# Kernel optimization log

Hardware: AMD Instinct MI355X
Metric: run time of the kernel (lower is better)

The kernel has to match this reference:

```python
import jax, jax.numpy as jnp
import numpy as np

N_HEADS = 8
N_LEVELS = 1
N_POINTS = 4
D_MODEL = 256
BATCH = 2
H0, W0 = 100, 150
LS = H0 * W0
LQ = 15000


def layer_norm(x, g, b, eps=1e-5):
    m = jnp.mean(x, -1, keepdims=True)
    v = jnp.var(x, -1, keepdims=True)
    return (x - m) * jax.lax.rsqrt(v + eps) * g + b


def bilinear_sample(v, Hl, Wl, loc):
    # v: [N, Hl*Wl, Hh, D] level features; loc in [0,1]: [N, Lq, Hh, P, 2] (x, y)
    Nb, _, Hh, D = v.shape
    Lq, P = loc.shape[1], loc.shape[3]
    x = loc[..., 0] * Wl - 0.5           # align_corners=False grid_sample convention
    y = loc[..., 1] * Hl - 0.5
    x0 = jnp.floor(x); y0 = jnp.floor(y)
    lx = (x - x0).transpose(0, 2, 1, 3)[..., None]   # [N,Hh,Lq,P,1]
    ly = (y - y0).transpose(0, 2, 1, 3)[..., None]
    x0i = x0.astype(jnp.int32); y0i = y0.astype(jnp.int32)
    vh = v.transpose(0, 2, 1, 3)                      # [N,Hh,Hl*Wl,D]

    def gather(xi, yi):
        valid = (xi >= 0) & (xi < Wl) & (yi >= 0) & (yi < Hl)   # zero padding
        idx = jnp.clip(yi, 0, Hl - 1) * Wl + jnp.clip(xi, 0, Wl - 1)
        idxf = idx.transpose(0, 2, 1, 3).reshape(Nb, Hh, Lq * P)
        g = jnp.take_along_axis(vh, idxf[..., None], axis=2).reshape(Nb, Hh, Lq, P, D)
        return g * valid.transpose(0, 2, 1, 3)[..., None]

    g00 = gather(x0i, y0i)
    g10 = gather(x0i + 1, y0i)
    g01 = gather(x0i, y0i + 1)
    g11 = gather(x0i + 1, y0i + 1)
    return (g00 * (1 - lx) * (1 - ly) + g10 * lx * (1 - ly)
            + g01 * (1 - lx) * ly + g11 * lx * ly)   # [N,Hh,Lq,P,D]


def ms_deform_attn(q, reference_points, src, shapes_np, starts_np, padding_mask,
                   W_val, b_val, W_off, b_off, W_attn, b_attn, W_out, b_out):
    Nb, Lq, C = q.shape
    Hh, D, L, P = N_HEADS, C // N_HEADS, N_LEVELS, N_POINTS
    value = src @ W_val + b_val
    value = jnp.where(padding_mask[..., None], 0.0, value).reshape(Nb, -1, Hh, D)
    offsets = (q @ W_off + b_off).reshape(Nb, Lq, Hh, L, P, 2)
    aw = jax.nn.softmax((q @ W_attn + b_attn).reshape(Nb, Lq, Hh, L * P), -1)
    aw = aw.reshape(Nb, Lq, Hh, L, P)
    # offset normalizer is (W, H) per level
    norm = jnp.asarray(shapes_np[:, ::-1].copy(), dtype=q.dtype)   # [L,2]
    loc = reference_points[:, :, None, :, None, :] + offsets / norm[None, None, None, :, None, :]
    out = 0.0
    for l in range(L):
        Hl, Wl = int(shapes_np[l, 0]), int(shapes_np[l, 1])
        s = int(starts_np[l])
        sampled = bilinear_sample(value[:, s:s + Hl * Wl], Hl, Wl, loc[:, :, :, l])
        out = out + jnp.sum(sampled * aw[:, :, :, l].transpose(0, 2, 1, 3)[..., None], axis=3)
    out = out.transpose(0, 2, 1, 3).reshape(Nb, Lq, C)
    return out @ W_out + b_out


def reference(tgt, query_pos, src_pos, tgt_spatial_shapes, reference_points,
              depth_reference_points, src, src_spatial_shapes, frame_start_index,
              src_padding_mask,
              W_dsa, b_dsa, g_nds, b_nds, W_off, b_off, W_attn, b_attn,
              W_val, b_val, W_out, b_out, W_csa, b_csa, g_n1, b_n1,
              W_ff, b_ff, g_n3, b_n3):
    ss = np.asarray(src_spatial_shapes)      # static level shapes
    starts = np.asarray(frame_start_index)
    # depth scale adaptation
    src_a = layer_norm(src @ W_dsa + b_dsa, g_nds, b_nds)
    q = tgt + query_pos
    tgt2 = ms_deform_attn(q, reference_points, src_a, ss, starts, src_padding_mask,
                          W_val, b_val, W_off, b_off, W_attn, b_attn, W_out, b_out)
    tgt2 = tgt2 @ W_csa + b_csa
    t = layer_norm(tgt + tgt2, g_n1, b_n1)
    # FFN: single linear d_model->d_model with exact GELU (per source code)
    ff = jax.nn.gelu(t @ W_ff + b_ff, approximate=False)
    return layer_norm(t + ff, g_n3, b_n3)


def setup_inputs() -> dict:
    key = jax.random.key(0)
    ks = jax.random.split(key, 24)
    C = D_MODEL
    Hh, L, P = N_HEADS, N_LEVELS, N_POINTS

    def lin(k, fin, fout, scale=None):
        s = (1.0 / np.sqrt(fin)) if scale is None else scale
        return (jax.random.normal(k, (fin, fout), jnp.float32) * s).astype(jnp.float32)

    inp = {}
    inp['tgt'] = jax.random.normal(ks[0], (BATCH, LQ, C), jnp.float32)
    inp['query_pos'] = 0.1 * jax.random.normal(ks[1], (BATCH, LQ, C), jnp.float32)
    inp['src_pos'] = 0.1 * jax.random.normal(ks[2], (BATCH, LS, C), jnp.float32)
    inp['tgt_spatial_shapes'] = jnp.array([[H0, W0]], jnp.int32)
    inp['reference_points'] = jax.random.uniform(ks[3], (BATCH, LQ, L, 2), jnp.float32)
    inp['depth_reference_points'] = jax.random.uniform(ks[4], (BATCH, LQ, 1, 2), jnp.float32)
    inp['src'] = jax.random.normal(ks[5], (BATCH, LS, C), jnp.float32)
    inp['src_spatial_shapes'] = jnp.array([[H0, W0]], jnp.int32)
    inp['frame_start_index'] = jnp.array([0], jnp.int32)
    inp['src_padding_mask'] = jnp.zeros((BATCH, LS), jnp.bool_)
    # parameters
    inp['W_dsa'] = lin(ks[6], C, C); inp['b_dsa'] = jnp.zeros((C,), jnp.float32)
    inp['g_nds'] = jnp.ones((C,), jnp.float32); inp['b_nds'] = jnp.zeros((C,), jnp.float32)
    inp['W_off'] = lin(ks[7], C, Hh * L * P * 2, scale=0.01)
    inp['b_off'] = 0.5 * jax.random.normal(ks[8], (Hh * L * P * 2,), jnp.float32)
    inp['W_attn'] = lin(ks[9], C, Hh * L * P)
    inp['b_attn'] = jnp.zeros((Hh * L * P,), jnp.float32)
    inp['W_val'] = lin(ks[10], C, C); inp['b_val'] = jnp.zeros((C,), jnp.float32)
    inp['W_out'] = lin(ks[11], C, C); inp['b_out'] = jnp.zeros((C,), jnp.float32)
    inp['W_csa'] = lin(ks[12], C, C); inp['b_csa'] = jnp.zeros((C,), jnp.float32)
    inp['g_n1'] = jnp.ones((C,), jnp.float32); inp['b_n1'] = jnp.zeros((C,), jnp.float32)
    inp['W_ff'] = lin(ks[13], C, C); inp['b_ff'] = jnp.zeros((C,), jnp.float32)
    inp['g_n3'] = jnp.ones((C,), jnp.float32); inp['b_n3'] = jnp.zeros((C,), jnp.float32)
    return inp
```

## Files before the change

### kernel.cpp

```cpp
#include <hip/hip_runtime.h>
#include <hip/hip_bf16.h>
#include <math.h>

#define LQ   15000
#define LS_  15000
#define NB   2
#define ROWS (NB*LQ)
#define HGT  100
#define WID  150

typedef __attribute__((ext_vector_type(8))) short bf16x8;
typedef __attribute__((ext_vector_type(4))) float f32x4;

__device__ inline short f2bf(float x) {
    __hip_bfloat16 h = __float2bfloat16(x);
    return *reinterpret_cast<short*>(&h);
}
__device__ inline unsigned pack2bf(float a, float b) {
    return ((unsigned)(unsigned short)f2bf(a)) | (((unsigned)(unsigned short)f2bf(b)) << 16);
}
__device__ inline float bf2f(short s) {
    return __uint_as_float(((unsigned)(unsigned short)s) << 16);
}
__device__ inline float gelu_exact(float x) {
    return 0.5f * x * (1.f + erff(x * 0.70710678118654752440f));
}

#if defined(__has_builtin)
#if __has_builtin(__builtin_amdgcn_global_load_lds)
#define HAS_GLL 1
#endif
#endif
#ifndef HAS_GLL
#define HAS_GLL 0
#endif

typedef unsigned int u32;

__device__ __forceinline__ void gld_lds16(const void* g, void* l) {
#if HAS_GLL
    __builtin_amdgcn_global_load_lds(
        (const __attribute__((address_space(1))) u32*)g,
        (__attribute__((address_space(3))) u32*)l,
        16, 0, 0);
#else
    int lane = threadIdx.x & 63;
    *(int4*)((char*)l + lane * 16) = *(const int4*)g;
#endif
}

#if HAS_GLL
#define WAIT_PREV() asm volatile("s_waitcnt vmcnt(4)" ::: "memory")
#define WAIT_LAST() asm volatile("s_waitcnt vmcnt(0)" ::: "memory")
#else
#define WAIT_PREV() asm volatile("s_waitcnt vmcnt(0) lgkmcnt(0)" ::: "memory")
#define WAIT_LAST() asm volatile("s_waitcnt vmcnt(0) lgkmcnt(0)" ::: "memory")
#endif

template<int MODE>
__global__ __launch_bounds__(256, 2) void fused2(
    const void* __restrict__ Ap,
    const short* __restrict__ W1T, const float* __restrict__ bias1,
    const float* __restrict__ res1,
    const float* __restrict__ g1v, const float* __restrict__ b1v,
    const short* __restrict__ W2T, const float* __restrict__ bias2,
    void* __restrict__ Out,
    const unsigned char* __restrict__ mask,
    const float* __restrict__ g2v, const float* __restrict__ b2v,
    int M)
{
    __shared__ __align__(16) char lds[2 * 16384 + 64 * 264 * 2];
    short (*T)[264] = (short(*)[264])(lds + 32768);

    const int tid = threadIdx.x;
    const int bm0 = blockIdx.x * 64;
    const int wave = tid >> 6, lane = tid & 63;
    const int quad = lane >> 4, c = lane & 15;

    const int roff = c * 64 + ((quad ^ ((c >> 1) & 3)) << 4);

    auto stageB = [&](int buf, const short* __restrict__ W, int k0) {
        #pragma unroll
        for (int it = 0; it < 4; ++it) {
            int s = it * 256 + wave * 64 + lane;
            int n = s >> 2;
            int j = (s & 3) ^ ((n >> 1) & 3);
            gld_lds16(W + (size_t)n * 256 + k0 + j * 8,
                      lds + buf * 16384 + (it * 256 + wave * 64) * 16);
        }
    };

    int rA = bm0 + wave * 16 + c; if (rA > M - 1) rA = M - 1;
    bf16x8 aReg[8];

    if (MODE == 1) {
        const short* A = (const short*)Ap + (size_t)rA * 256 + quad * 8;
        #pragma unroll
        for (int k = 0; k < 8; ++k) aReg[k] = *(const bf16x8*)(A + k * 32);
    } else {
        const float* A = (const float*)Ap + (size_t)rA * 256 + quad * 8;
        float4 lo[8], hi[8];
        #pragma unroll
        for (int k = 0; k < 8; ++k) {
            lo[k] = *(const float4*)(A + k * 32);
            hi[k] = *(const float4*)(A + k * 32 + 4);
        }
        #pragma unroll
        for (int k = 0; k < 8; ++k) {
            union { int4 i; bf16x8 v; } u;
            u.i.x = pack2bf(lo[k].x, lo[k].y);
            u.i.y = pack2bf(lo[k].z, lo[k].w);
            u.i.z = pack2bf(hi[k].x, hi[k].y);
            u.i.w = pack2bf(hi[k].z, hi[k].w);
            aReg[k] = u.v;
        }
    }

    stageB(0, W1T, 0);
    stageB(1, W1T, 32);

    f32x4 acc[16];
    #pragma unroll
    for (int t = 0; t < 16; ++t) acc[t] = (f32x4){0.f, 0.f, 0.f, 0.f};

    #pragma unroll
    for (int k = 0; k < 8; ++k) {
        if (k < 7) { WAIT_PREV(); } else { WAIT_LAST(); }
        __builtin_amdgcn_s_barrier();
        const char* bb = lds + (k & 1) * 16384 + roff;
        bf16x8 a = aReg[k];
        #pragma unroll
        for (int t = 0; t < 16; ++t) {
            bf16x8 b = *(const bf16x8*)(bb + t * 1024);
            acc[t] = __builtin_amdgcn_mfma_f32_16x16x32_bf16(a, b, acc[t], 0, 0, 0);
        }
        asm volatile("" ::: "memory");
        __builtin_amdgcn_s_barrier();
        if (k < 6) stageB(k & 1, W1T, (k + 2) * 32);
    }

    stageB(0, W2T, 0);
    stageB(1, W2T, 32);

    float tres[4][16];
    {
        const int rb = wave * 16 + quad * 4;
        #pragma unroll
        for (int reg = 0; reg < 4; ++reg) {
            int rloc = rb + reg;
            int rg = bm0 + rloc; int rgl = (rg < M) ? rg : (M - 1);
            float s = 0.f, sq = 0.f;
            float vv[16];
            #pragma unroll
            for (int t = 0; t < 16; ++t) {
                int col = t * 16 + c;
                float v = acc[t][reg] + bias1[col];
                if (MODE == 1) v += res1[(size_t)rgl * 256 + col];
                vv[t] = v; s += v; sq += v * v;
            }
            #pragma unroll
            for (int o = 1; o < 16; o <<= 1) {
                s += __shfl_xor(s, o, 64); sq += __shfl_xor(sq, o, 64);
            }
            float mean = s * (1.f / 256.f);
            float var  = sq * (1.f / 256.f) - mean * mean;
            float rs   = rsqrtf(var + 1e-5f);
            #pragma unroll
            for (int t = 0; t < 16; ++t) {
                int col = t * 16 + c;
                float ln = (vv[t] - mean) * rs * g1v[col] + b1v[col];
                if (MODE == 1) tres[reg][t] = ln;
                T[rloc][col] = f2bf(ln);
            }
        }
    }

    #pragma unroll
    for (int k = 0; k < 8; ++k)
        aReg[k] = *(const bf16x8*)&T[wave * 16 + c][k * 32 + quad * 8];

    #pragma unroll
    for (int t = 0; t < 16; ++t) acc[t] = (f32x4){0.f, 0.f, 0.f, 0.f};

    #pragma unroll
    for (int k = 0; k < 8; ++k) {
        if (k < 7) { WAIT_PREV(); } else { WAIT_LAST(); }
        __builtin_amdgcn_s_barrier();
        const char* bb = lds + (k & 1) * 16384 + roff;
        bf16x8 a = aReg[k];
        #pragma unroll
        for (int t = 0; t < 16; ++t) {
            bf16x8 b = *(const bf16x8*)(bb + t * 1024);
            acc[t] = __builtin_amdgcn_mfma_f32_16x16x32_bf16(a, b, acc[t], 0, 0, 0);
        }
        asm volatile("" ::: "memory");
        __builtin_amdgcn_s_barrier();
        if (k < 6) stageB(k & 1, W2T, (k + 2) * 32);
    }

    const int rb = wave * 16 + quad * 4;
    if constexpr (MODE == 0) {
        short* O = (short*)Out;
        #pragma unroll
        for (int reg = 0; reg < 4; ++reg) {
            int rloc = rb + reg; int r = bm0 + rloc;
            if (r < M) {
                float mz = mask[r] ? 0.f : 1.f;
                int n = (r >= LS_) ? 1 : 0;
                int sidx = r - n * LS_;
                #pragma unroll
                for (int t = 0; t < 16; ++t) {
                    int col = t * 16 + c; int h = col >> 5, d = col & 31;
                    O[(((size_t)n * 8 + h) * LS_ + sidx) * 32 + d] =
                        f2bf((acc[t][reg] + bias2[col]) * mz);
                }
            }
        }
    } else {
        float* O = (float*)Out;
        #pragma unroll
        for (int reg = 0; reg < 4; ++reg) {
            int r = bm0 + rb + reg;
            float s = 0.f, sq = 0.f;
            float vv[16];
            #pragma unroll
            for (int t = 0; t < 16; ++t) {
                int col = t * 16 + c;
                float v = gelu_exact(acc[t][reg] + bias2[col]) + tres[reg][t];
                vv[t] = v; s += v; sq += v * v;
            }
            #pragma unroll
            for (int o = 1; o < 16; o <<= 1) {
                s += __shfl_xor(s, o, 64); sq += __shfl_xor(sq, o, 64);
            }
            float mean = s * (1.f / 256.f);
            float var  = sq * (1.f / 256.f) - mean * mean;
            float rs   = rsqrtf(var + 1e-5f);
            if (r < M) {
                #pragma unroll
                for (int t = 0; t < 16; ++t) {
                    int col = t * 16 + c;
                    O[(size_t)r * 256 + col] = (vv[t] - mean) * rs * g2v[col] + b2v[col];
                }
            }
        }
    }
}

__global__ __launch_bounds__(256) void oa_gemm(
    const float* __restrict__ tgt, const float* __restrict__ qpos,
    const short* __restrict__ WToa, const float* __restrict__ b_oa,
    float* __restrict__ S_oa, int M)
{
    __shared__ __align__(16) short Bs[96][264];
    __shared__ float sb[96];

    const int tid = threadIdx.x;
    const int bm0 = blockIdx.x * 64;
    const int wave = tid >> 6, lane = tid & 63;
    const int quad = lane >> 4, c = lane & 15;

    if (tid < 96) sb[tid] = b_oa[tid];

    #pragma unroll
    for (int it = 0; it < 12; ++it) {
        int f = it * 256 + tid;
        int n = f >> 5, ko = (f & 31) * 8;
        *(int4*)&Bs[n][ko] = *(const int4*)&WToa[(size_t)n * 256 + ko];
    }

    int r = bm0 + wave * 16 + c; if (r > M - 1) r = M - 1;
    const float* At = tgt  + (size_t)r * 256 + quad * 8;
    const float* Aq = qpos + (size_t)r * 256 + quad * 8;
    bf16x8 aReg[8];
    #pragma unroll
    for (int k = 0; k < 8; ++k) {
        float4 t0 = *(const float4*)(At + k * 32);
        float4 t1 = *(const float4*)(At + k * 32 + 4);
        float4 q0 = *(const float4*)(Aq + k * 32);
        float4 q1 = *(const float4*)(Aq + k * 32 + 4);
        union { int4 i; bf16x8 v; } u;
        u.i.x = pack2bf(t0.x + q0.x, t0.y + q0.y);
        u.i.y = pack2bf(t0.z + q0.z, t0.w + q0.w);
        u.i.z = pack2bf(t1.x + q1.x, t1.y + q1.y);
        u.i.w = pack2bf(t1.z + q1.z, t1.w + q1.w);
        aReg[k] = u.v;
    }

    f32x4 acc[6];
    #pragma unroll
    for (int t = 0; t < 6; ++t) acc[t] = (f32x4){0.f, 0.f, 0.f, 0.f};

    __syncthreads();

    #pragma unroll
    for (int k = 0; k < 8; ++k) {
        bf16x8 a = aReg[k];
        #pragma unroll
        for (int t = 0; t < 6; ++t) {
            bf16x8 b = *(const bf16x8*)&Bs[t * 16 + c][k * 32 + quad * 8];
            acc[t] = __builtin_amdgcn_mfma_f32_16x16x32_bf16(a, b, acc[t], 0, 0, 0);
        }
    }

    const int rb = wave * 16 + quad * 4;
    #pragma unroll
    for (int reg = 0; reg < 4; ++reg) {
        int rr = bm0 + rb + reg;
        if (rr < M) {
            #pragma unroll
            for (int t = 0; t < 6; ++t)
                S_oa[(size_t)rr * 96 + t * 16 + c] = acc[t][reg] + sb[t * 16 + c];
        }
    }
}

__global__ __launch_bounds__(256) void deform_sample(
    const short* __restrict__ value,
    const float* __restrict__ S_oa,
    const float* __restrict__ refp,
    short* __restrict__ out)
{
    int grp = blockIdx.x * 32 + (threadIdx.x >> 3);
    int c4  = threadIdx.x & 7;
    int h = grp & 7;
    int r = grp >> 3;
    int n = (r >= LS_) ? 1 : 0;

    const float* row = S_oa + (size_t)r * 96;
    float rx = refp[(size_t)r * 2 + 0], ry = refp[(size_t)r * 2 + 1];
    float4 oA = *(const float4*)&row[h * 8];
    float4 oB = *(const float4*)&row[h * 8 + 4];
    float4 lg = *(const float4*)&row[64 + h * 4];

    float mx = fmaxf(fmaxf(lg.x, lg.y), fmaxf(lg.z, lg.w));
    float e0 = expf(lg.x - mx), e1 = expf(lg.y - mx), e2 = expf(lg.z - mx), e3 = expf(lg.w - mx);
    float inv = 1.f / (e0 + e1 + e2 + e3);
    float aw[4] = {e0 * inv, e1 * inv, e2 * inv, e3 * inv};
    float ox[4] = {oA.x, oA.z, oB.x, oB.z};
    float oy[4] = {oA.y, oA.w, oB.y, oB.w};

    const short* vb = value + (((size_t)n * 8 + h) * LS_) * 32 + c4 * 4;
    float a0 = 0.f, a1 = 0.f, a2 = 0.f, a3 = 0.f;

    #pragma unroll
    for (int p = 0; p < 4; ++p) {
        float x = rx * (float)WID + ox[p] - 0.5f;
        float y = ry * (float)HGT + oy[p] - 0.5f;
        float x0f = floorf(x), y0f = floorf(y);
        float lx = x - x0f, ly = y - y0f;
        int x0 = (int)x0f, y0 = (int)y0f;
        int x1 = x0 + 1, y1 = y0 + 1;
        bool vx0 = (x0 >= 0) & (x0 < WID), vx1 = (x1 >= 0) & (x1 < WID);
        bool vy0 = (y0 >= 0) & (y0 < HGT), vy1 = (y1 >= 0) & (y1 < HGT);
        float w00 = (vx0 & vy0) ? (1.f - lx) * (1.f - ly) * aw[p] : 0.f;
        float w10 = (vx1 & vy0) ? lx * (1.f - ly) * aw[p] : 0.f;
        float w01 = (vx0 & vy1) ? (1.f - lx) * ly * aw[p] : 0.f;
        float w11 = (vx1 & vy1) ? lx * ly * aw[p] : 0.f;
        int xc0 = min(max(x0, 0), WID - 1), xc1 = min(max(x1, 0), WID - 1);
        int yc0 = min(max(y0, 0), HGT - 1), yc1 = min(max(y1, 0), HGT - 1);
        int2 v00 = *(const int2*)&vb[(size_t)(yc0 * WID + xc0) * 32];
        int2 v10 = *(const int2*)&vb[(size_t)(yc0 * WID + xc1) * 32];
        int2 v01 = *(const int2*)&vb[(size_t)(yc1 * WID + xc0) * 32];
        int2 v11 = *(const int2*)&vb[(size_t)(yc1 * WID + xc1) * 32];
        a0 += w00 * __uint_as_float(((unsigned)v00.x) << 16)
            + w10 * __uint_as_float(((unsigned)v10.x) << 16)
            + w01 * __uint_as_float(((unsigned)v01.x) << 16)
            + w11 * __uint_as_float(((unsigned)v11.x) << 16);
        a1 += w00 * __uint_as_float(v00.x & 0xffff0000u)
            + w10 * __uint_as_float(v10.x & 0xffff0000u)
            + w01 * __uint_as_float(v01.x & 0xffff0000u)
            + w11 * __uint_as_float(v11.x & 0xffff0000u);
        a2 += w00 * __uint_as_float(((unsigned)v00.y) << 16)
            + w10 * __uint_as_float(((unsigned)v10.y) << 16)
            + w01 * __uint_as_float(((unsigned)v01.y) << 16)
            + w11 * __uint_as_float(((unsigned)v11.y) << 16);
        a3 += w00 * __uint_as_float(v00.y & 0xffff0000u)
            + w10 * __uint_as_float(v10.y & 0xffff0000u)
            + w01 * __uint_as_float(v01.y & 0xffff0000u)
            + w11 * __uint_as_float(v11.y & 0xffff0000u);
    }
    int2 o;
    o.x = pack2bf(a0, a1);
    o.y = pack2bf(a2, a3);
    *(int2*)&out[(size_t)r * 256 + h * 32 + c4 * 4] = o;
}

__global__ __launch_bounds__(256) void prep_all(
    const float* __restrict__ W_dsa, const float* __restrict__ W_val,
    const float* __restrict__ W_ff,  const float* __restrict__ W_out,
    const float* __restrict__ W_csa, const float* __restrict__ b_out,
    const float* __restrict__ b_csa, const float* __restrict__ W_off,
    const float* __restrict__ W_attn, const float* __restrict__ b_off,
    const float* __restrict__ b_attn,
    short* __restrict__ WT_dsa, short* __restrict__ WT_val, short* __restrict__ WT_ff,
    short* __restrict__ WT_c, float* __restrict__ bc,
    short* __restrict__ WT_oa, float* __restrict__ b_oa)
{
    __shared__ float tile[64][65];
    const int b = blockIdx.x, tid = threadIdx.x;
    if (b < 48) {
        const float* W = (b < 16) ? W_dsa : (b < 32) ? W_val : W_ff;
        short* WT = (b < 16) ? WT_dsa : (b < 32) ? WT_val : WT_ff;
        int t = b & 15; int bx = (t & 3) * 64, by = (t >> 2) * 64;
        #pragma unroll
        for (int it = 0; it < 4; ++it) {
            int f = it * 256 + tid; int i = f >> 4; int j = (f & 15) * 4;
            float4 v = *(const float4*)&W[(size_t)(by + i) * 256 + bx + j];
            tile[i][j] = v.x; tile[i][j + 1] = v.y; tile[i][j + 2] = v.z; tile[i][j + 3] = v.w;
        }
        __syncthreads();
        #pragma unroll
        for (int it = 0; it < 16; ++it) {
            int f = it * 256 + tid; int nl = f >> 6; int kl = f & 63;
            WT[(size_t)(bx + nl) * 256 + by + kl] = f2bf(tile[kl][nl]);
        }
    } else if (b < 304) {
        int k = b - 48, n = tid;
        float s = 0.f;
        #pragma unroll 8
        for (int j = 0; j < 256; ++j)
            s = fmaf(W_out[(size_t)k * 256 + j], W_csa[(size_t)j * 256 + n], s);
        WT_c[(size_t)n * 256 + k] = f2bf(s);
    } else if (b == 304) {
        int j = tid;
        float s = b_csa[j];
        #pragma unroll 8
        for (int k = 0; k < 256; ++k)
            s = fmaf(b_out[k], W_csa[(size_t)k * 256 + j], s);
        bc[j] = s;
    } else {
        int j = b - 305, k = tid;
        float v = (j < 64) ? W_off[(size_t)k * 64 + j] : W_attn[(size_t)k * 32 + (j - 64)];
        WT_oa[(size_t)j * 256 + k] = f2bf(v);
        if (k == 0) b_oa[j] = (j < 64) ? b_off[j] : b_attn[j - 64];
    }
}

extern "C" void kernel_launch(void* const* d_in, const int* in_sizes, int n_in,
                              void* d_out, int out_size, void* d_ws, size_t ws_size,
                              hipStream_t stream)
{
    const float* tgt       = (const float*)d_in[0];
    const float* query_pos = (const float*)d_in[1];
    const float* refp      = (const float*)d_in[4];
    const float* src       = (const float*)d_in[6];
    const unsigned char* mask = (const unsigned char*)d_in[9];
    const float* W_dsa  = (const float*)d_in[10]; const float* b_dsa  = (const float*)d_in[11];
    const float* g_nds  = (const float*)d_in[12]; const float* b_nds  = (const float*)d_in[13];
    const float* W_off  = (const float*)d_in[14]; const float* b_off  = (const float*)d_in[15];
    const float* W_attn = (const float*)d_in[16]; const float* b_attn = (const float*)d_in[17];
    const float* W_val  = (const float*)d_in[18]; const float* b_val  = (const float*)d_in[19];
    const float* W_out  = (const float*)d_in[20]; const float* b_out  = (const float*)d_in[21];
    const float* W_csa  = (const float*)d_in[22]; const float* b_csa  = (const float*)d_in[23];
    const float* g_n1   = (const float*)d_in[24]; const float* b_n1   = (const float*)d_in[25];
    const float* W_ff   = (const float*)d_in[26]; const float* b_ff   = (const float*)d_in[27];
    const float* g_n3   = (const float*)d_in[28]; const float* b_n3   = (const float*)d_in[29];
    float* out = (float*)d_out;

    short* attn_out = (short*)d_ws;
    short* value    = attn_out + (size_t)ROWS * 256;
    float* S_oa     = (float*)(value + (size_t)ROWS * 256);
    short* WT_dsa   = (short*)(S_oa + (size_t)ROWS * 96);
    short* WT_val   = WT_dsa + 65536;
    short* WT_ff    = WT_val + 65536;
    short* WT_c     = WT_ff + 65536;
    short* WT_oa    = WT_c + 65536;
    float* bc       = (float*)(WT_oa + 96 * 256);
    float* b_oa     = bc + 256;

    dim3 blk(256);
    const int GB = (ROWS + 63) / 64;

    prep_all<<<401, blk, 0, stream>>>(
        W_dsa, W_val, W_ff, W_out, W_csa, b_out, b_csa, W_off, W_attn, b_off, b_attn,
        WT_dsa, WT_val, WT_ff, WT_c, bc, WT_oa, b_oa);

    oa_gemm<<<GB, blk, 0, stream>>>(tgt, query_pos, WT_oa, b_oa, S_oa, ROWS);

    fused2<0><<<GB, blk, 0, stream>>>(
        src, WT_dsa, b_dsa, nullptr, g_nds, b_nds,
        WT_val, b_val, value, mask, nullptr, nullptr, ROWS);

    deform_sample<<<ROWS * 8 / 32, blk, 0, stream>>>(value, S_oa, refp, attn_out);

    fused2<1><<<GB, blk, 0, stream>>>(
        attn_out, WT_c, bc, tgt, g_n1, b_n1,
        WT_ff, b_ff, out, nullptr, g_n3, b_n3, ROWS);
}
```

Measured before the change: 298.1 us.

## Split fused2 columns across 8 waves to halve accumulator registers

The fused two-GEMM kernel now runs with 512 threads, where pairs of waves share 16 rows and each handles half of the 256 output columns. Each wave keeps 8 accumulators instead of 16, the goal being lower register pressure and more resident waves. The LayerNorm row statistics are combined through a small LDS partials array. The residual for MODE 1 is re-read as bf16 from the T tile instead of being held in fp32 registers. In exchange it adds more __syncthreads barriers, replaces the explicit vmcnt waits with full barriers, slightly changes residual precision, and uses more LDS per block, which may cap how many blocks fit.

New measurement: 293.2 us. Within noise of the previous version (-1.6%).

```diff
diff --git a/kernel.cpp b/kernel.cpp
--- a/kernel.cpp
+++ b/kernel.cpp
@@ -49,16 +49,8 @@
 #endif
 }
 
-#if HAS_GLL
-#define WAIT_PREV() asm volatile("s_waitcnt vmcnt(4)" ::: "memory")
-#define WAIT_LAST() asm volatile("s_waitcnt vmcnt(0)" ::: "memory")
-#else
-#define WAIT_PREV() asm volatile("s_waitcnt vmcnt(0) lgkmcnt(0)" ::: "memory")
-#define WAIT_LAST() asm volatile("s_waitcnt vmcnt(0) lgkmcnt(0)" ::: "memory")
-#endif
-
 template<int MODE>
-__global__ __launch_bounds__(256, 2) void fused2(
+__global__ __launch_bounds__(512, 4) void fused2(
     const void* __restrict__ Ap,
     const short* __restrict__ W1T, const float* __restrict__ bias1,
     const float* __restrict__ res1,
@@ -69,28 +61,31 @@
     const float* __restrict__ g2v, const float* __restrict__ b2v,
     int M)
 {
-    __shared__ __align__(16) char lds[2 * 16384 + 64 * 264 * 2];
+    __shared__ __align__(16) char lds[2 * 16384 + 64 * 264 * 2 + 1024];
     short (*T)[264] = (short(*)[264])(lds + 32768);
+    float (*PR)[2][2] = (float(*)[2][2])(lds + 66560);
 
     const int tid = threadIdx.x;
     const int bm0 = blockIdx.x * 64;
     const int wave = tid >> 6, lane = tid & 63;
     const int quad = lane >> 4, c = lane & 15;
+    const int p = wave >> 1, h = wave & 1;
+    const int rowbase = p * 16;
 
     const int roff = c * 64 + ((quad ^ ((c >> 1) & 3)) << 4);
 
     auto stageB = [&](int buf, const short* __restrict__ W, int k0) {
         #pragma unroll
-        for (int it = 0; it < 4; ++it) {
-            int s = it * 256 + wave * 64 + lane;
+        for (int it = 0; it < 2; ++it) {
+            int s = it * 512 + wave * 64 + lane;
             int n = s >> 2;
             int j = (s & 3) ^ ((n >> 1) & 3);
             gld_lds16(W + (size_t)n * 256 + k0 + j * 8,
-                      lds + buf * 16384 + (it * 256 + wave * 64) * 16);
+                      lds + buf * 16384 + (it * 512 + wave * 64) * 16);
         }
     };
 
-    int rA = bm0 + wave * 16 + c; if (rA > M - 1) rA = M - 1;
+    int rA = bm0 + rowbase + c; if (rA > M - 1) rA = M - 1;
     bf16x8 aReg[8];
 
     if (MODE == 1) {
@@ -99,148 +94,150 @@
         for (int k = 0; k < 8; ++k) aReg[k] = *(const bf16x8*)(A + k * 32);
     } else {
         const float* A = (const float*)Ap + (size_t)rA * 256 + quad * 8;
-        float4 lo[8], hi[8];
         #pragma unroll
         for (int k = 0; k < 8; ++k) {
-            lo[k] = *(const float4*)(A + k * 32);
-            hi[k] = *(const float4*)(A + k * 32 + 4);
-        }
-        #pragma unroll
-        for (int k = 0; k < 8; ++k) {
+            float4 lo = *(const float4*)(A + k * 32);
+            float4 hi = *(const float4*)(A + k * 32 + 4);
             union { int4 i; bf16x8 v; } u;
-            u.i.x = pack2bf(lo[k].x, lo[k].y);
-            u.i.y = pack2bf(lo[k].z, lo[k].w);
-            u.i.z = pack2bf(hi[k].x, hi[k].y);
-            u.i.w = pack2bf(hi[k].z, hi[k].w);
+            u.i.x = pack2bf(lo.x, lo.y);
+            u.i.y = pack2bf(lo.z, lo.w);
+            u.i.z = pack2bf(hi.x, hi.y);
+            u.i.w = pack2bf(hi.z, hi.w);
             aReg[k] = u.v;
         }
     }
 
     stageB(0, W1T, 0);
-    stageB(1, W1T, 32);
-
-    f32x4 acc[16];
-    #pragma unroll
-    for (int t = 0; t < 16; ++t) acc[t] = (f32x4){0.f, 0.f, 0.f, 0.f};
+
+    f32x4 acc[8];
+    #pragma unroll
+    for (int t = 0; t < 8; ++t) acc[t] = (f32x4){0.f, 0.f, 0.f, 0.f};
+
+    __syncthreads();
 
     #pragma unroll
     for (int k = 0; k < 8; ++k) {
-        if (k < 7) { WAIT_PREV(); } else { WAIT_LAST(); }
-        __builtin_amdgcn_s_barrier();
-        const char* bb = lds + (k & 1) * 16384 + roff;
+        if (k < 7) stageB((k + 1) & 1, W1T, (k + 1) * 32);
+        const char* bb = lds + (k & 1) * 16384 + h * 8192 + roff;
         bf16x8 a = aReg[k];
         #pragma unroll
-        for (int t = 0; t < 16; ++t) {
+        for (int t = 0; t < 8; ++t) {
             bf16x8 b = *(const bf16x8*)(bb + t * 1024);
             acc[t] = __builtin_amdgcn_mfma_f32_16x16x32_bf16(a, b, acc[t], 0, 0, 0);
         }
-        asm volatile("" ::: "memory");
-        __builtin_amdgcn_s_barrier();
-        if (k < 6) stageB(k & 1, W1T, (k + 2) * 32);
+        __syncthreads();
     }
 
     stageB(0, W2T, 0);
-    stageB(1, W2T, 32);
-
-    float tres[4][16];
+
     {
-        const int rb = wave * 16 + quad * 4;
+        float vv[4][8];
         #pragma unroll
         for (int reg = 0; reg < 4; ++reg) {
-            int rloc = rb + reg;
+            int rloc = rowbase + quad * 4 + reg;
             int rg = bm0 + rloc; int rgl = (rg < M) ? rg : (M - 1);
             float s = 0.f, sq = 0.f;
-            float vv[16];
-            #pragma unroll
-            for (int t = 0; t < 16; ++t) {
-                int col = t * 16 + c;
+            #pragma unroll
+            for (int t = 0; t < 8; ++t) {
+                int col = h * 128 + t * 16 + c;
                 float v = acc[t][reg] + bias1[col];
                 if (MODE == 1) v += res1[(size_t)rgl * 256 + col];
-                vv[t] = v; s += v; sq += v * v;
+                vv[reg][t] = v; s += v; sq += v * v;
             }
             #pragma unroll
             for (int o = 1; o < 16; o <<= 1) {
                 s += __shfl_xor(s, o, 64); sq += __shfl_xor(sq, o, 64);
             }
+            if (c == 0) { PR[rloc][h][0] = s; PR[rloc][h][1] = sq; }
+        }
+        __syncthreads();
+        #pragma unroll
+        for (int reg = 0; reg < 4; ++reg) {
+            int rloc = rowbase + quad * 4 + reg;
+            float s  = PR[rloc][0][0] + PR[rloc][1][0];
+            float sq = PR[rloc][0][1] + PR[rloc][1][1];
             float mean = s * (1.f / 256.f);
             float var  = sq * (1.f / 256.f) - mean * mean;
             float rs   = rsqrtf(var + 1e-5f);
             #pragma unroll
-            for (int t = 0; t < 16; ++t) {
-                int col = t * 16 + c;
-                float ln = (vv[t] - mean) * rs * g1v[col] + b1v[col];
-                if (MODE == 1) tres[reg][t] = ln;
-                T[rloc][col] = f2bf(ln);
-            }
-        }
+            for (int t = 0; t < 8; ++t) {
+                int col = h * 128 + t * 16 + c;
+                T[rloc][col] = f2bf((vv[reg][t] - mean) * rs * g1v[col] + b1v[col]);
+            }
+        }
+        __syncthreads();
     }
 
     #pragma unroll
     for (int k = 0; k < 8; ++k)
-        aReg[k] = *(const bf16x8*)&T[wave * 16 + c][k * 32 + quad * 8];
-
-    #pragma unroll
-    for (int t = 0; t < 16; ++t) acc[t] = (f32x4){0.f, 0.f, 0.f, 0.f};
+        aReg[k] = *(const bf16x8*)&T[rowbase + c][k * 32 + quad * 8];
+
+    #pragma unroll
+    for (int t = 0; t < 8; ++t) acc[t] = (f32x4){0.f, 0.f, 0.f, 0.f};
 
     #pragma unroll
     for (int k = 0; k < 8; ++k) {
-        if (k < 7) { WAIT_PREV(); } else { WAIT_LAST(); }
-        __builtin_amdgcn_s_barrier();
-        const char* bb = lds + (k & 1) * 16384 + roff;
+        if (k < 7) stageB((k + 1) & 1, W2T, (k + 1) * 32);
+        const char* bb = lds + (k & 1) * 16384 + h * 8192 + roff;
         bf16x8 a = aReg[k];
         #pragma unroll
-        for (int t = 0; t < 16; ++t) {
+        for (int t = 0; t < 8; ++t) {
             bf16x8 b = *(const bf16x8*)(bb + t * 1024);
             acc[t] = __builtin_amdgcn_mfma_f32_16x16x32_bf16(a, b, acc[t], 0, 0, 0);
         }
-        asm volatile("" ::: "memory");
-        __builtin_amdgcn_s_barrier();
-        if (k < 6) stageB(k & 1, W2T, (k + 2) * 32);
-    }
-
-    const int rb = wave * 16 + quad * 4;
+        __syncthreads();
+    }
+
     if constexpr (MODE == 0) {
         short* O = (short*)Out;
         #pragma unroll
         for (int reg = 0; reg < 4; ++reg) {
-            int rloc = rb + reg; int r = bm0 + rloc;
+            int rloc = rowbase + quad * 4 + reg; int r = bm0 + rloc;
             if (r < M) {
                 float mz = mask[r] ? 0.f : 1.f;
                 int n = (r >= LS_) ? 1 : 0;
                 int sidx = r - n * LS_;
                 #pragma unroll
-                for (int t = 0; t < 16; ++t) {
-                    int col = t * 16 + c; int h = col >> 5, d = col & 31;
-                    O[(((size_t)n * 8 + h) * LS_ + sidx) * 32 + d] =
+                for (int t = 0; t < 8; ++t) {
+                    int col = h * 128 + t * 16 + c; int hh = col >> 5, d = col & 31;
+                    O[(((size_t)n * 8 + hh) * LS_ + sidx) * 32 + d] =
                         f2bf((acc[t][reg] + bias2[col]) * mz);
                 }
             }
         }
     } else {
         float* O = (float*)Out;
+        float vv[4][8];
         #pragma unroll
         for (int reg = 0; reg < 4; ++reg) {
-            int r = bm0 + rb + reg;
+            int rloc = rowbase + quad * 4 + reg;
             float s = 0.f, sq = 0.f;
-            float vv[16];
-            #pragma unroll
-            for (int t = 0; t < 16; ++t) {
-                int col = t * 16 + c;
-                float v = gelu_exact(acc[t][reg] + bias2[col]) + tres[reg][t];
-                vv[t] = v; s += v; sq += v * v;
+            #pragma unroll
+            for (int t = 0; t < 8; ++t) {
+                int col = h * 128 + t * 16 + c;
+                float v = gelu_exact(acc[t][reg] + bias2[col]) + bf2f(T[rloc][col]);
+                vv[reg][t] = v; s += v; sq += v * v;
             }
             #pragma unroll
             for (int o = 1; o < 16; o <<= 1) {
                 s += __shfl_xor(s, o, 64); sq += __shfl_xor(sq, o, 64);
             }
+            if (c == 0) { PR[rloc][h][0] = s; PR[rloc][h][1] = sq; }
+        }
+        __syncthreads();
+        #pragma unroll
+        for (int reg = 0; reg < 4; ++reg) {
+            int rloc = rowbase + quad * 4 + reg; int r = bm0 + rloc;
+            float s  = PR[rloc][0][0] + PR[rloc][1][0];
+            float sq = PR[rloc][0][1] + PR[rloc][1][1];
             float mean = s * (1.f / 256.f);
             float var  = sq * (1.f / 256.f) - mean * mean;
             float rs   = rsqrtf(var + 1e-5f);
             if (r < M) {
                 #pragma unroll
-                for (int t = 0; t < 16; ++t) {
-                    int col = t * 16 + c;
-                    O[(size_t)r * 256 + col] = (vv[t] - mean) * rs * g2v[col] + b2v[col];
+                for (int t = 0; t < 8; ++t) {
+                    int col = h * 128 + t * 16 + c;
+                    O[(size_t)r * 256 + col] = (vv[reg][t] - mean) * rs * g2v[col] + b2v[col];
                 }
             }
         }
@@ -469,7 +466,7 @@
     float* bc       = (float*)(WT_oa + 96 * 256);
     float* b_oa     = bc + 256;
 
-    dim3 blk(256);
+    dim3 blk(256), blk2(512);
     const int GB = (ROWS + 63) / 64;
 
     prep_all<<<401, blk, 0, stream>>>(
@@ -478,13 +475,13 @@
 
     oa_gemm<<<GB, blk, 0, stream>>>(tgt, query_pos, WT_oa, b_oa, S_oa, ROWS);
 
-    fused2<0><<<GB, blk, 0, stream>>>(
+    fused2<0><<<GB, blk2, 0, stream>>>(
         src, WT_dsa, b_dsa, nullptr, g_nds, b_nds,
         WT_val, b_val, value, mask, nullptr, nullptr, ROWS);
 
     deform_sample<<<ROWS * 8 / 32, blk, 0, stream>>>(value, S_oa, refp, attn_out);
 
-    fused2<1><<<GB, blk, 0, stream>>>(
+    fused2<1><<<GB, blk2, 0, stream>>>(
         attn_out, WT_c, bc, tgt, g_n1, b_n1,
         WT_ff, b_ff, out, nullptr, g_n3, b_n3, ROWS);
 }
```

## Shrink fused GEMM blocks to 128 threads and simplify B-tile pipeline

Applied to the files above, without the earlier changes.

The fused two-GEMM kernel now runs with 2 waves per block covering 32 rows instead of 4 waves covering 64, which doubles the grid and cuts LDS per block. The weight-staging loop is reworked into a one-ahead prefetch with __syncthreads in place of hand-placed vmcnt waits and raw barriers. The fp32 A-load conversion is interleaved per k-step to reduce live registers. Each block now re-stages the full weight tiles for half as many rows, doubling weight traffic per row, and the looser waits may expose more load latency.

After: 332.5 us. 1.12x slower.

```diff
diff --git a/kernel.cpp b/kernel.cpp
--- a/kernel.cpp
+++ b/kernel.cpp
@@ -49,16 +49,8 @@
 #endif
 }
 
-#if HAS_GLL
-#define WAIT_PREV() asm volatile("s_waitcnt vmcnt(4)" ::: "memory")
-#define WAIT_LAST() asm volatile("s_waitcnt vmcnt(0)" ::: "memory")
-#else
-#define WAIT_PREV() asm volatile("s_waitcnt vmcnt(0) lgkmcnt(0)" ::: "memory")
-#define WAIT_LAST() asm volatile("s_waitcnt vmcnt(0) lgkmcnt(0)" ::: "memory")
-#endif
-
 template<int MODE>
-__global__ __launch_bounds__(256, 2) void fused2(
+__global__ __launch_bounds__(128, 2) void fused2(
     const void* __restrict__ Ap,
     const short* __restrict__ W1T, const float* __restrict__ bias1,
     const float* __restrict__ res1,
@@ -69,11 +61,11 @@
     const float* __restrict__ g2v, const float* __restrict__ b2v,
     int M)
 {
-    __shared__ __align__(16) char lds[2 * 16384 + 64 * 264 * 2];
+    __shared__ __align__(16) char lds[2 * 16384 + 32 * 264 * 2];
     short (*T)[264] = (short(*)[264])(lds + 32768);
 
     const int tid = threadIdx.x;
-    const int bm0 = blockIdx.x * 64;
+    const int bm0 = blockIdx.x * 32;
     const int wave = tid >> 6, lane = tid & 63;
     const int quad = lane >> 4, c = lane & 15;
 
@@ -81,12 +73,13 @@
 
     auto stageB = [&](int buf, const short* __restrict__ W, int k0) {
         #pragma unroll
-        for (int it = 0; it < 4; ++it) {
-            int s = it * 256 + wave * 64 + lane;
+        for (int it = 0; it < 8; ++it) {
+            int sbase = it * 128 + wave * 64;
+            int s = sbase + lane;
             int n = s >> 2;
             int j = (s & 3) ^ ((n >> 1) & 3);
             gld_lds16(W + (size_t)n * 256 + k0 + j * 8,
-                      lds + buf * 16384 + (it * 256 + wave * 64) * 16);
+                      lds + buf * 16384 + sbase * 16);
         }
     };
 
@@ -99,34 +92,30 @@
         for (int k = 0; k < 8; ++k) aReg[k] = *(const bf16x8*)(A + k * 32);
     } else {
         const float* A = (const float*)Ap + (size_t)rA * 256 + quad * 8;
-        float4 lo[8], hi[8];
         #pragma unroll
         for (int k = 0; k < 8; ++k) {
-            lo[k] = *(const float4*)(A + k * 32);
-            hi[k] = *(const float4*)(A + k * 32 + 4);
-        }
-        #pragma unroll
-        for (int k = 0; k < 8; ++k) {
+            float4 lo = *(const float4*)(A + k * 32);
+            float4 hi = *(const float4*)(A + k * 32 + 4);
             union { int4 i; bf16x8 v; } u;
-            u.i.x = pack2bf(lo[k].x, lo[k].y);
-            u.i.y = pack2bf(lo[k].z, lo[k].w);
-            u.i.z = pack2bf(hi[k].x, hi[k].y);
-            u.i.w = pack2bf(hi[k].z, hi[k].w);
+            u.i.x = pack2bf(lo.x, lo.y);
+            u.i.y = pack2bf(lo.z, lo.w);
+            u.i.z = pack2bf(hi.x, hi.y);
+            u.i.w = pack2bf(hi.z, hi.w);
             aReg[k] = u.v;
         }
     }
 
     stageB(0, W1T, 0);
-    stageB(1, W1T, 32);
 
     f32x4 acc[16];
     #pragma unroll
     for (int t = 0; t < 16; ++t) acc[t] = (f32x4){0.f, 0.f, 0.f, 0.f};
 
+    __syncthreads();
+
     #pragma unroll
     for (int k = 0; k < 8; ++k) {
-        if (k < 7) { WAIT_PREV(); } else { WAIT_LAST(); }
-        __builtin_amdgcn_s_barrier();
+        if (k < 7) stageB((k + 1) & 1, W1T, (k + 1) * 32);
         const char* bb = lds + (k & 1) * 16384 + roff;
         bf16x8 a = aReg[k];
         #pragma unroll
@@ -134,13 +123,10 @@
             bf16x8 b = *(const bf16x8*)(bb + t * 1024);
             acc[t] = __builtin_amdgcn_mfma_f32_16x16x32_bf16(a, b, acc[t], 0, 0, 0);
         }
-        asm volatile("" ::: "memory");
-        __builtin_amdgcn_s_barrier();
-        if (k < 6) stageB(k & 1, W1T, (k + 2) * 32);
+        __syncthreads();
     }
 
     stageB(0, W2T, 0);
-    stageB(1, W2T, 32);
 
     float tres[4][16];
     {
@@ -182,10 +168,11 @@
     #pragma unroll
     for (int t = 0; t < 16; ++t) acc[t] = (f32x4){0.f, 0.f, 0.f, 0.f};
 
+    __syncthreads();
+
     #pragma unroll
     for (int k = 0; k < 8; ++k) {
-        if (k < 7) { WAIT_PREV(); } else { WAIT_LAST(); }
-        __builtin_amdgcn_s_barrier();
+        if (k < 7) stageB((k + 1) & 1, W2T, (k + 1) * 32);
         const char* bb = lds + (k & 1) * 16384 + roff;
         bf16x8 a = aReg[k];
         #pragma unroll
@@ -193,9 +180,7 @@
             bf16x8 b = *(const bf16x8*)(bb + t * 1024);
             acc[t] = __builtin_amdgcn_mfma_f32_16x16x32_bf16(a, b, acc[t], 0, 0, 0);
         }
-        asm volatile("" ::: "memory");
-        __builtin_amdgcn_s_barrier();
-        if (k < 6) stageB(k & 1, W2T, (k + 2) * 32);
+        __syncthreads();
     }
 
     const int rb = wave * 16 + quad * 4;
@@ -469,8 +454,9 @@
     float* bc       = (float*)(WT_oa + 96 * 256);
     float* b_oa     = bc + 256;
 
-    dim3 blk(256);
-    const int GB = (ROWS + 63) / 64;
+    dim3 blk(256), blkf(128);
+    const int GB  = (ROWS + 63) / 64;
+    const int GB2 = (ROWS + 31) / 32;
 
     prep_all<<<401, blk, 0, stream>>>(
         W_dsa, W_val, W_ff, W_out, W_csa, b_out, b_csa, W_off, W_attn, b_off, b_attn,
@@ -478,13 +464,13 @@
 
     oa_gemm<<<GB, blk, 0, stream>>>(tgt, query_pos, WT_oa, b_oa, S_oa, ROWS);
 
-    fused2<0><<<GB, blk, 0, stream>>>(
+    fused2<0><<<GB2, blkf, 0, stream>>>(
         src, WT_dsa, b_dsa, nullptr, g_nds, b_nds,
         WT_val, b_val, value, mask, nullptr, nullptr, ROWS);
 
     deform_sample<<<ROWS * 8 / 32, blk, 0, stream>>>(value, S_oa, refp, attn_out);
 
-    fused2<1><<<GB, blk, 0, stream>>>(
+    fused2<1><<<GB2, blkf, 0, stream>>>(
         attn_out, WT_c, bc, tgt, g_n1, b_n1,
         WT_ff, b_ff, out, nullptr, g_n3, b_n3, ROWS);
 }
```

## Widen deform sampler loads to 16 bytes; simplify GEMM B-tile staging sync

Applied to the files above, without the earlier changes.

The deformable sampler now gives each thread 8 channels instead of 4. It uses 16-byte gathers and stores, which halves the thread count and the duplicated offset and softmax work per (row, head). Separately, fused2's double-buffered B staging now issues the next tile load at the start of each k step and uses __syncthreads, replacing the explicit vmcnt waits that kept two tiles in flight. This is simpler but may expose more load latency, because only one tile is prefetched at a time.

After: 296.3 us. Within noise of the previous version (-0.6%).

```diff
diff --git a/kernel.cpp b/kernel.cpp
--- a/kernel.cpp
+++ b/kernel.cpp
@@ -22,6 +22,8 @@
 __device__ inline float bf2f(short s) {
     return __uint_as_float(((unsigned)(unsigned short)s) << 16);
 }
+__device__ inline float lo16(int w) { return __uint_as_float(((unsigned)w) << 16); }
+__device__ inline float hi16(int w) { return __uint_as_float(((unsigned)w) & 0xffff0000u); }
 __device__ inline float gelu_exact(float x) {
     return 0.5f * x * (1.f + erff(x * 0.70710678118654752440f));
 }
@@ -48,14 +50,6 @@
     *(int4*)((char*)l + lane * 16) = *(const int4*)g;
 #endif
 }
-
-#if HAS_GLL
-#define WAIT_PREV() asm volatile("s_waitcnt vmcnt(4)" ::: "memory")
-#define WAIT_LAST() asm volatile("s_waitcnt vmcnt(0)" ::: "memory")
-#else
-#define WAIT_PREV() asm volatile("s_waitcnt vmcnt(0) lgkmcnt(0)" ::: "memory")
-#define WAIT_LAST() asm volatile("s_waitcnt vmcnt(0) lgkmcnt(0)" ::: "memory")
-#endif
 
 template<int MODE>
 __global__ __launch_bounds__(256, 2) void fused2(
@@ -117,16 +111,16 @@
     }
 
     stageB(0, W1T, 0);
-    stageB(1, W1T, 32);
 
     f32x4 acc[16];
     #pragma unroll
     for (int t = 0; t < 16; ++t) acc[t] = (f32x4){0.f, 0.f, 0.f, 0.f};
 
+    __syncthreads();
+
     #pragma unroll
     for (int k = 0; k < 8; ++k) {
-        if (k < 7) { WAIT_PREV(); } else { WAIT_LAST(); }
-        __builtin_amdgcn_s_barrier();
+        if (k < 7) stageB((k + 1) & 1, W1T, (k + 1) * 32);
         const char* bb = lds + (k & 1) * 16384 + roff;
         bf16x8 a = aReg[k];
         #pragma unroll
@@ -134,13 +128,10 @@
             bf16x8 b = *(const bf16x8*)(bb + t * 1024);
             acc[t] = __builtin_amdgcn_mfma_f32_16x16x32_bf16(a, b, acc[t], 0, 0, 0);
         }
-        asm volatile("" ::: "memory");
-        __builtin_amdgcn_s_barrier();
-        if (k < 6) stageB(k & 1, W1T, (k + 2) * 32);
+        __syncthreads();
     }
 
     stageB(0, W2T, 0);
-    stageB(1, W2T, 32);
 
     float tres[4][16];
     {
@@ -182,10 +173,11 @@
     #pragma unroll
     for (int t = 0; t < 16; ++t) acc[t] = (f32x4){0.f, 0.f, 0.f, 0.f};
 
+    __syncthreads();
+
     #pragma unroll
     for (int k = 0; k < 8; ++k) {
-        if (k < 7) { WAIT_PREV(); } else { WAIT_LAST(); }
-        __builtin_amdgcn_s_barrier();
+        if (k < 7) stageB((k + 1) & 1, W2T, (k + 1) * 32);
         const char* bb = lds + (k & 1) * 16384 + roff;
         bf16x8 a = aReg[k];
         #pragma unroll
@@ -193,9 +185,7 @@
             bf16x8 b = *(const bf16x8*)(bb + t * 1024);
             acc[t] = __builtin_amdgcn_mfma_f32_16x16x32_bf16(a, b, acc[t], 0, 0, 0);
         }
-        asm volatile("" ::: "memory");
-        __builtin_amdgcn_s_barrier();
-        if (k < 6) stageB(k & 1, W2T, (k + 2) * 32);
+        __syncthreads();
     }
 
     const int rb = wave * 16 + quad * 4;
@@ -321,8 +311,8 @@
     const float* __restrict__ refp,
     short* __restrict__ out)
 {
-    int grp = blockIdx.x * 32 + (threadIdx.x >> 3);
-    int c4  = threadIdx.x & 7;
+    int grp = blockIdx.x * 64 + (threadIdx.x >> 2);
+    int c4  = threadIdx.x & 3;
     int h = grp & 7;
     int r = grp >> 3;
     int n = (r >= LS_) ? 1 : 0;
@@ -340,8 +330,9 @@
     float ox[4] = {oA.x, oA.z, oB.x, oB.z};
     float oy[4] = {oA.y, oA.w, oB.y, oB.w};
 
-    const short* vb = value + (((size_t)n * 8 + h) * LS_) * 32 + c4 * 4;
+    const short* vb = value + (((size_t)n * 8 + h) * LS_) * 32 + c4 * 8;
     float a0 = 0.f, a1 = 0.f, a2 = 0.f, a3 = 0.f;
+    float a4 = 0.f, a5 = 0.f, a6 = 0.f, a7 = 0.f;
 
     #pragma unroll
     for (int p = 0; p < 4; ++p) {
@@ -359,31 +350,25 @@
         float w11 = (vx1 & vy1) ? lx * ly * aw[p] : 0.f;
         int xc0 = min(max(x0, 0), WID - 1), xc1 = min(max(x1, 0), WID - 1);
         int yc0 = min(max(y0, 0), HGT - 1), yc1 = min(max(y1, 0), HGT - 1);
-        int2 v00 = *(const int2*)&vb[(size_t)(yc0 * WID + xc0) * 32];
-        int2 v10 = *(const int2*)&vb[(size_t)(yc0 * WID + xc1) * 32];
-        int2 v01 = *(const int2*)&vb[(size_t)(yc1 * WID + xc0) * 32];
-        int2 v11 = *(const int2*)&vb[(size_t)(yc1 * WID + xc1) * 32];
-        a0 += w00 * __uint_as_float(((unsigned)v00.x) << 16)
-            + w10 * __uint_as_float(((unsigned)v10.x) << 16)
-            + w01 * __uint_as_float(((unsigned)v01.x) << 16)
-            + w11 * __uint_as_float(((unsigned)v11.x) << 16);
-        a1 += w00 * __uint_as_float(v00.x & 0xffff0000u)
-            + w10 * __uint_as_float(v10.x & 0xffff0000u)
-            + w01 * __uint_as_float(v01.x & 0xffff0000u)
-            + w11 * __uint_as_float(v11.x & 0xffff0000u);
-        a2 += w00 * __uint_as_float(((unsigned)v00.y) << 16)
-            + w10 * __uint_as_float(((unsigned)v10.y) << 16)
-            + w01 * __uint_as_float(((unsigned)v01.y) << 16)
-            + w11 * __uint_as_float(((unsigned)v11.y) << 16);
-        a3 += w00 * __uint_as_float(v00.y & 0xffff0000u)
-            + w10 * __uint_as_float(v10.y & 0xffff0000u)
-            + w01 * __uint_as_float(v01.y & 0xffff0000u)
-            + w11 * __uint_as_float(v11.y & 0xffff0000u);
-    }
-    int2 o;
+        int4 v00 = *(const int4*)&vb[(size_t)(yc0 * WID + xc0) * 32];
+        int4 v10 = *(const int4*)&vb[(size_t)(yc0 * WID + xc1) * 32];
+        int4 v01 = *(const int4*)&vb[(size_t)(yc1 * WID + xc0) * 32];
+        int4 v11 = *(const int4*)&vb[(size_t)(yc1 * WID + xc1) * 32];
+        a0 += w00 * lo16(v00.x) + w10 * lo16(v10.x) + w01 * lo16(v01.x) + w11 * lo16(v11.x);
+        a1 += w00 * hi16(v00.x) + w10 * hi16(v10.x) + w01 * hi16(v01.x) + w11 * hi16(v11.x);
+        a2 += w00 * lo16(v00.y) + w10 * lo16(v10.y) + w01 * lo16(v01.y) + w11 * lo16(v11.y);
+        a3 += w00 * hi16(v00.y) + w10 * hi16(v10.y) + w01 * hi16(v01.y) + w11 * hi16(v11.y);
+        a4 += w00 * lo16(v00.z) + w10 * lo16(v10.z) + w01 * lo16(v01.z) + w11 * lo16(v11.z);
+        a5 += w00 * hi16(v00.z) + w10 * hi16(v10.z) + w01 * hi16(v01.z) + w11 * hi16(v11.z);
+        a6 += w00 * lo16(v00.w) + w10 * lo16(v10.w) + w01 * lo16(v01.w) + w11 * lo16(v11.w);
+        a7 += w00 * hi16(v00.w) + w10 * hi16(v10.w) + w01 * hi16(v01.w) + w11 * hi16(v11.w);
+    }
+    int4 o;
     o.x = pack2bf(a0, a1);
     o.y = pack2bf(a2, a3);
-    *(int2*)&out[(size_t)r * 256 + h * 32 + c4 * 4] = o;
+    o.z = pack2bf(a4, a5);
+    o.w = pack2bf(a6, a7);
+    *(int4*)&out[(size_t)r * 256 + h * 32 + c4 * 8] = o;
 }
 
 __global__ __launch_bounds__(256) void prep_all(
@@ -482,7 +467,7 @@
         src, WT_dsa, b_dsa, nullptr, g_nds, b_nds,
         WT_val, b_val, value, mask, nullptr, nullptr, ROWS);
 
-    deform_sample<<<ROWS * 8 / 32, blk, 0, stream>>>(value, S_oa, refp, attn_out);
+    deform_sample<<<ROWS * 8 / 64, blk, 0, stream>>>(value, S_oa, refp, attn_out);
 
     fused2<1><<<GB, blk, 0, stream>>>(
         attn_out, WT_c, bc, tgt, g_n1, b_n1,
```
